# Kernel optimization log

Hardware: AMD Instinct MI355X
Metric: run time of the kernel (lower is better)

The kernel has to match this reference:

```python
import jax, jax.numpy as jnp
import numpy as np

N, E = 50000, 800000
NODE_DIM, EDGE_DIM, H = 64, 32, 128


def setup_inputs() -> dict:
    key = jax.random.key(0)
    ks = jax.random.split(key, 12)
    s = lambda fan_in: 1.0 / np.sqrt(fan_in)
    return {
        "node_feat": jax.random.normal(ks[0], (N, NODE_DIM), dtype=jnp.float32),
        "edge_index": jax.random.randint(ks[1], (2, E), 0, N, dtype=jnp.int32),
        "edge_feat": jax.random.normal(ks[2], (E, EDGE_DIM), dtype=jnp.float32),
        # node_proj: Linear(node_dim -> H)
        "W_node": jax.random.uniform(ks[3], (H, NODE_DIM), jnp.float32, -s(NODE_DIM), s(NODE_DIM)),
        "b_node": jnp.zeros((H,), jnp.float32),
        # edge_proj: Linear(edge_dim -> H)
        "W_edge": jax.random.uniform(ks[4], (H, EDGE_DIM), jnp.float32, -s(EDGE_DIM), s(EDGE_DIM)),
        "b_edge": jnp.zeros((H,), jnp.float32),
        # message: Linear(2H -> H)
        "W_msg": jax.random.uniform(ks[5], (H, 2 * H), jnp.float32, -s(2 * H), s(2 * H)),
        "b_msg": jnp.zeros((H,), jnp.float32),
        # GRUCell(H, H): weight_ih [3H,H], weight_hh [3H,H], biases [3H]
        "W_ih": jax.random.uniform(ks[6], (3 * H, H), jnp.float32, -s(H), s(H)),
        "W_hh": jax.random.uniform(ks[7], (3 * H, H), jnp.float32, -s(H), s(H)),
        "b_ih": jax.random.uniform(ks[8], (3 * H,), jnp.float32, -s(H), s(H)),
        "b_hh": jax.random.uniform(ks[9], (3 * H,), jnp.float32, -s(H), s(H)),
    }


def _gru_cell(x, h, W_ih, W_hh, b_ih, b_hh):
    # torch.nn.GRUCell semantics; gate order: reset, update, new
    gi = x @ W_ih.T + b_ih   # [N, 3H]
    gh = h @ W_hh.T + b_hh   # [N, 3H]
    i_r, i_z, i_n = jnp.split(gi, 3, axis=-1)
    h_r, h_z, h_n = jnp.split(gh, 3, axis=-1)
    r = jax.nn.sigmoid(i_r + h_r)
    z = jax.nn.sigmoid(i_z + h_z)
    n = jnp.tanh(i_n + r * h_n)
    return (1.0 - z) * n + z * h


def reference(node_feat, edge_index, edge_feat, W_node, b_node, W_edge, b_edge,
              W_msg, b_msg, W_ih, W_hh, b_ih, b_hh):
    h = node_feat @ W_node.T + b_node          # [N, H]
    e = edge_feat @ W_edge.T + b_edge          # [E, H]
    src, dst = edge_index[0], edge_index[1]
    n_nodes = h.shape[0]
    # Split the message Linear over the concat to avoid materializing [E, 2H]
    W_msg_h, W_msg_e = W_msg[:, :h.shape[1]], W_msg[:, h.shape[1]:]
    e_msg = e @ W_msg_e.T + b_msg              # edge part is loop-invariant
    for _ in range(3):
        m = h[src] @ W_msg_h.T + e_msg         # [E, H]
        agg = jax.ops.segment_sum(m, dst, num_segments=n_nodes)  # [N, H]
        h = _gru_cell(agg, h, W_ih, W_hh, b_ih, b_hh)
    return (h, e)
```

## Files before the change

kernel.cpp:

```cpp
#include <hip/hip_runtime.h>
#include <hip/hip_bf16.h>

#define NN 50000
#define EE 800000
#define ND 64
#define ED 32
#define HH 128

template<int KSTEP, bool BIAS, bool CMAT, bool DEGB>
__global__ __launch_bounds__(256) void k_gemm(
    const float* __restrict__ X, int K,
    const float* __restrict__ W, int ldw,
    const float* __restrict__ bias,
    const float* __restrict__ Cm,
    const int* __restrict__ deg,
    float* __restrict__ Y, int M, int Ncols)
{
    __shared__ float Xs[64][KSTEP + 1];
    __shared__ float Ws[64][KSTEP + 1];
    const int m0 = blockIdx.x * 64;
    const int n0 = blockIdx.y * 64;
    const int tid = threadIdx.x;
    const int tx = tid & 15, ty = tid >> 4;

    float acc[4][4] = {};

    for (int k0 = 0; k0 < K; k0 += KSTEP) {
        for (int f = tid; f < 64 * KSTEP / 4; f += 256) {
            int r = f / (KSTEP / 4);
            int c4 = (f % (KSTEP / 4)) * 4;
            int gr = m0 + r;
            float4 v = make_float4(0.f, 0.f, 0.f, 0.f);
            if (gr < M)
                v = *reinterpret_cast<const float4*>(X + (size_t)gr * K + k0 + c4);
            Xs[r][c4 + 0] = v.x; Xs[r][c4 + 1] = v.y;
            Xs[r][c4 + 2] = v.z; Xs[r][c4 + 3] = v.w;
        }
        for (int f = tid; f < 64 * KSTEP / 4; f += 256) {
            int r = f / (KSTEP / 4);
            int c4 = (f % (KSTEP / 4)) * 4;
            float4 v = *reinterpret_cast<const float4*>(W + (size_t)(n0 + r) * ldw + k0 + c4);
            Ws[r][c4 + 0] = v.x; Ws[r][c4 + 1] = v.y;
            Ws[r][c4 + 2] = v.z; Ws[r][c4 + 3] = v.w;
        }
        __syncthreads();
        #pragma unroll
        for (int kk = 0; kk < KSTEP; ++kk) {
            float a[4], b[4];
            #pragma unroll
            for (int i = 0; i < 4; ++i) a[i] = Xs[ty * 4 + i][kk];
            #pragma unroll
            for (int j = 0; j < 4; ++j) b[j] = Ws[tx * 4 + j][kk];
            #pragma unroll
            for (int i = 0; i < 4; ++i)
                #pragma unroll
                for (int j = 0; j < 4; ++j)
                    acc[i][j] += a[i] * b[j];
        }
        __syncthreads();
    }

    #pragma unroll
    for (int i = 0; i < 4; ++i) {
        int row = m0 + ty * 4 + i;
        if (row >= M) continue;
        #pragma unroll
        for (int j = 0; j < 4; ++j) {
            int col = n0 + tx * 4 + j;
            float v = acc[i][j];
            if (BIAS) v += DEGB ? bias[col] * (float)deg[row] : bias[col];
            if (CMAT) v += Cm[(size_t)row * Ncols + col];
            Y[(size_t)row * Ncols + col] = v;
        }
    }
}

__global__ __launch_bounds__(256) void k_gru(
    const float* __restrict__ hin, const float* __restrict__ Whh,
    const float* __restrict__ bhh, const float* __restrict__ gi,
    float* __restrict__ hout, int M)
{
    constexpr int KS = 32;
    __shared__ float Hs[64][KS + 1];
    __shared__ float Wr[64][KS + 1];
    __shared__ float Wz[64][KS + 1];
    __shared__ float Wn[64][KS + 1];
    const int m0 = blockIdx.x * 64;
    const int c0 = blockIdx.y * 64;
    const int tid = threadIdx.x;
    const int tx = tid & 15, ty = tid >> 4;

    float ar[4][4] = {}, az[4][4] = {}, an[4][4] = {};

    for (int k0 = 0; k0 < HH; k0 += KS) {
        for (int f = tid; f < 64 * KS / 4; f += 256) {
            int r = f / (KS / 4);
            int c4 = (f % (KS / 4)) * 4;
            int gr = m0 + r;
            float4 v = make_float4(0.f, 0.f, 0.f, 0.f);
            if (gr < M)
                v = *reinterpret_cast<const float4*>(hin + (size_t)gr * HH + k0 + c4);
            Hs[r][c4] = v.x; Hs[r][c4 + 1] = v.y; Hs[r][c4 + 2] = v.z; Hs[r][c4 + 3] = v.w;

            float4 w0 = *reinterpret_cast<const float4*>(Whh + (size_t)(c0 + r) * HH + k0 + c4);
            Wr[r][c4] = w0.x; Wr[r][c4 + 1] = w0.y; Wr[r][c4 + 2] = w0.z; Wr[r][c4 + 3] = w0.w;
            float4 w1 = *reinterpret_cast<const float4*>(Whh + (size_t)(HH + c0 + r) * HH + k0 + c4);
            Wz[r][c4] = w1.x; Wz[r][c4 + 1] = w1.y; Wz[r][c4 + 2] = w1.z; Wz[r][c4 + 3] = w1.w;
            float4 w2 = *reinterpret_cast<const float4*>(Whh + (size_t)(2 * HH + c0 + r) * HH + k0 + c4);
            Wn[r][c4] = w2.x; Wn[r][c4 + 1] = w2.y; Wn[r][c4 + 2] = w2.z; Wn[r][c4 + 3] = w2.w;
        }
        __syncthreads();
        #pragma unroll
        for (int kk = 0; kk < KS; ++kk) {
            float a[4], br[4], bz[4], bn[4];
            #pragma unroll
            for (int i = 0; i < 4; ++i) a[i] = Hs[ty * 4 + i][kk];
            #pragma unroll
            for (int j = 0; j < 4; ++j) {
                br[j] = Wr[tx * 4 + j][kk];
                bz[j] = Wz[tx * 4 + j][kk];
                bn[j] = Wn[tx * 4 + j][kk];
            }
            #pragma unroll
            for (int i = 0; i < 4; ++i)
                #pragma unroll
                for (int j = 0; j < 4; ++j) {
                    ar[i][j] += a[i] * br[j];
                    az[i][j] += a[i] * bz[j];
                    an[i][j] += a[i] * bn[j];
                }
        }
        __syncthreads();
    }

    #pragma unroll
    for (int i = 0; i < 4; ++i) {
        int row = m0 + ty * 4 + i;
        if (row >= M) continue;
        #pragma unroll
        for (int j = 0; j < 4; ++j) {
            int c = c0 + tx * 4 + j;
            float gr_ = gi[(size_t)row * 384 + c];
            float gz_ = gi[(size_t)row * 384 + HH + c];
            float gn_ = gi[(size_t)row * 384 + 2 * HH + c];
            float hr = ar[i][j] + bhh[c];
            float hz = az[i][j] + bhh[HH + c];
            float hn = an[i][j] + bhh[2 * HH + c];
            float r = 1.f / (1.f + expf(-(gr_ + hr)));
            float z = 1.f / (1.f + expf(-(gz_ + hz)));
            float n = tanhf(gn_ + r * hn);
            float hv = hin[(size_t)row * HH + c];
            hout[(size_t)row * HH + c] = (1.f - z) * n + z * hv;
        }
    }
}

__global__ void k_hist(const int* __restrict__ dst, int* __restrict__ deg, int n) {
    int e = blockIdx.x * 256 + threadIdx.x;
    if (e < n) atomicAdd(&deg[dst[e]], 1);
}

__global__ __launch_bounds__(1024) void k_scan_block(
    const int* __restrict__ deg, int* __restrict__ rp, int* __restrict__ bsum, int n)
{
    __shared__ int s[1024];
    int i = blockIdx.x * 1024 + threadIdx.x;
    s[threadIdx.x] = (i < n) ? deg[i] : 0;
    __syncthreads();
    for (int off = 1; off < 1024; off <<= 1) {
        int t = (threadIdx.x >= (unsigned)off) ? s[threadIdx.x - off] : 0;
        __syncthreads();
        s[threadIdx.x] += t;
        __syncthreads();
    }
    if (i < n) rp[i + 1] = s[threadIdx.x];
    if (threadIdx.x == 1023) bsum[blockIdx.x] = s[1023];
}

__global__ void k_scan_tops(int* bsum, int nb) {
    if (threadIdx.x == 0 && blockIdx.x == 0) {
        int run = 0;
        for (int b = 0; b < nb; ++b) { int v = bsum[b]; bsum[b] = run; run += v; }
    }
}

__global__ __launch_bounds__(1024) void k_scan_add(int* rp, const int* __restrict__ bsum, int n) {
    int i = blockIdx.x * 1024 + threadIdx.x;
    if (i < n) rp[i + 1] += bsum[blockIdx.x];
    if (i == 0) rp[0] = 0;
}

__global__ void k_cursor(const int* __restrict__ rp, int* __restrict__ cur, int n) {
    int i = blockIdx.x * 256 + threadIdx.x;
    if (i < n) cur[i] = rp[i];
}

__global__ void k_bucket(const int* __restrict__ src, const int* __restrict__ dst,
                         int* __restrict__ cur, int* __restrict__ eid,
                         int* __restrict__ ssrc, int n)
{
    int e = blockIdx.x * 256 + threadIdx.x;
    if (e < n) {
        int d = dst[e];
        int p = atomicAdd(&cur[d], 1);
        eid[p] = e;
        ssrc[p] = src[e];
    }
}

__global__ __launch_bounds__(256) void k_pull(
    const float* __restrict__ X, const int* __restrict__ idxarr,
    const int* __restrict__ rp, float* __restrict__ out, int n)
{
    int node = blockIdx.x * 4 + (threadIdx.x >> 6);
    int lane = threadIdx.x & 63;
    if (node >= n) return;
    int s = rp[node], t = rp[node + 1];
    float2 acc = make_float2(0.f, 0.f);
    for (int j = s; j < t; ++j) {
        int id = idxarr[j];
        float2 v = reinterpret_cast<const float2*>(X + (size_t)id * HH)[lane];
        acc.x += v.x; acc.y += v.y;
    }
    reinterpret_cast<float2*>(out + (size_t)node * HH)[lane] = acc;
}

extern "C" void kernel_launch(void* const* d_in, const int* in_sizes, int n_in,
                              void* d_out, int out_size, void* d_ws, size_t ws_size,
                              hipStream_t stream)
{
    const float* node_feat = (const float*)d_in[0];
    const int*   eidx      = (const int*)d_in[1];
    const float* edge_feat = (const float*)d_in[2];
    const float* W_node    = (const float*)d_in[3];
    const float* b_node    = (const float*)d_in[4];
    const float* W_edge    = (const float*)d_in[5];
    const float* b_edge    = (const float*)d_in[6];
    const float* W_msg     = (const float*)d_in[7];
    const float* b_msg     = (const float*)d_in[8];
    const float* W_ih      = (const float*)d_in[9];
    const float* W_hh      = (const float*)d_in[10];
    const float* b_ih      = (const float*)d_in[11];
    const float* b_hh      = (const float*)d_in[12];

    const int* src = eidx;
    const int* dst = eidx + EE;

    float* out_h = (float*)d_out;
    float* out_e = out_h + (size_t)NN * HH;

    float* A   = (float*)d_ws;
    float* B   = A + (size_t)NN * HH;
    float* C   = B + (size_t)NN * HH;
    float* D   = C + (size_t)NN * HH;
    float* Eb  = D + (size_t)NN * HH;
    float* F   = Eb + (size_t)NN * HH;
    int* deg   = (int*)(F + (size_t)NN * 384);
    int* rp    = deg + NN;
    int* cur   = rp + (NN + 1);
    int* bsum  = cur + NN;
    int* eid   = bsum + 64;
    int* ssrc  = eid + EE;

    hipMemsetAsync(deg, 0, NN * sizeof(int), stream);

    k_gemm<32, true, false, false><<<dim3(782, 2), 256, 0, stream>>>(
        node_feat, ND, W_node, ND, b_node, nullptr, nullptr, A, NN, HH);

    k_gemm<32, true, false, false><<<dim3(12500, 2), 256, 0, stream>>>(
        edge_feat, ED, W_edge, ED, b_edge, nullptr, nullptr, out_e, EE, HH);

    k_hist<<<EE / 256, 256, 0, stream>>>(dst, deg, EE);
    k_scan_block<<<49, 1024, 0, stream>>>(deg, rp, bsum, NN);
    k_scan_tops<<<1, 64, 0, stream>>>(bsum, 49);
    k_scan_add<<<49, 1024, 0, stream>>>(rp, bsum, NN);
    k_cursor<<<196, 256, 0, stream>>>(rp, cur, NN);
    k_bucket<<<EE / 256, 256, 0, stream>>>(src, dst, cur, eid, ssrc, EE);

    k_pull<<<12500, 256, 0, stream>>>(out_e, eid, rp, D, NN);
    k_gemm<32, true, false, true><<<dim3(782, 2), 256, 0, stream>>>(
        D, HH, W_msg + HH, 2 * HH, b_msg, nullptr, deg, C, NN, HH);

    const float* hin = A;
    for (int t = 0; t < 3; ++t) {
        float* hout = (t == 2) ? out_h : ((t == 0) ? B : A);
        k_pull<<<12500, 256, 0, stream>>>(hin, ssrc, rp, D, NN);
        k_gemm<32, false, true, false><<<dim3(782, 2), 256, 0, stream>>>(
            D, HH, W_msg, 2 * HH, nullptr, C, nullptr, Eb, NN, HH);
        k_gemm<32, true, false, false><<<dim3(782, 6), 256, 0, stream>>>(
            Eb, HH, W_ih, HH, b_ih, nullptr, nullptr, F, NN, 384);
        k_gru<<<dim3(782, 2), 256, 0, stream>>>(hin, W_hh, b_hh, F, hout, NN);
        hin = hout;
    }
}
```

Before: 1.984 ms.

## Replace FP32 SIMT GEMMs with split-bf16 MFMA GEMMs and restructure the GRU

Replaces the scalar FP32 tiled GEMM and the dedicated GRU kernel with one 128x128-tile MFMA GEMM. Each operand is split into bf16 high and low parts and three bf16 MFMAs are accumulated, approximating FP32 accuracy on matrix cores. The GRU now runs as an MFMA GEMM that adds the r/z hidden gates into F, then an n-gate GEMM with a fused sigmoid/tanh epilogue that writes h. The aim is to cut the ALU-bound GEMM cost, at the price of split-precision rounding error, an extra launch per iteration, and in-place updates of F and A whose safety depends on the access pattern (row blocks only touch their own rows).

```diff
diff --git a/kernel.cpp b/kernel.cpp
--- a/kernel.cpp
+++ b/kernel.cpp
@@ -7,150 +7,156 @@
 #define ED 32
 #define HH 128
 
-template<int KSTEP, bool BIAS, bool CMAT, bool DEGB>
-__global__ __launch_bounds__(256) void k_gemm(
+typedef __attribute__((ext_vector_type(8)))  short  bf16x8;
+typedef __attribute__((ext_vector_type(4)))  float  f32x4;
+typedef __attribute__((ext_vector_type(8)))  ushort u16x8;
+
+__device__ __forceinline__ ushort f2bf(float f) {
+    unsigned u = __float_as_uint(f);
+    unsigned r = (u + 0x7FFFu + ((u >> 16) & 1u)) >> 16;
+    return (ushort)r;
+}
+__device__ __forceinline__ float bf2f(ushort h) {
+    return __uint_as_float(((unsigned)h) << 16);
+}
+
+template<bool BIAS, bool CMAT, bool DEGB, bool GRU>
+__global__ __launch_bounds__(256) void k_mgemm(
     const float* __restrict__ X, int K,
     const float* __restrict__ W, int ldw,
     const float* __restrict__ bias,
-    const float* __restrict__ Cm,
+    const float* __restrict__ Cm, int ldc,
     const int* __restrict__ deg,
-    float* __restrict__ Y, int M, int Ncols)
-{
-    __shared__ float Xs[64][KSTEP + 1];
-    __shared__ float Ws[64][KSTEP + 1];
-    const int m0 = blockIdx.x * 64;
-    const int n0 = blockIdx.y * 64;
-    const int tid = threadIdx.x;
-    const int tx = tid & 15, ty = tid >> 4;
-
-    float acc[4][4] = {};
-
-    for (int k0 = 0; k0 < K; k0 += KSTEP) {
-        for (int f = tid; f < 64 * KSTEP / 4; f += 256) {
-            int r = f / (KSTEP / 4);
-            int c4 = (f % (KSTEP / 4)) * 4;
-            int gr = m0 + r;
-            float4 v = make_float4(0.f, 0.f, 0.f, 0.f);
-            if (gr < M)
-                v = *reinterpret_cast<const float4*>(X + (size_t)gr * K + k0 + c4);
-            Xs[r][c4 + 0] = v.x; Xs[r][c4 + 1] = v.y;
-            Xs[r][c4 + 2] = v.z; Xs[r][c4 + 3] = v.w;
-        }
-        for (int f = tid; f < 64 * KSTEP / 4; f += 256) {
-            int r = f / (KSTEP / 4);
-            int c4 = (f % (KSTEP / 4)) * 4;
-            float4 v = *reinterpret_cast<const float4*>(W + (size_t)(n0 + r) * ldw + k0 + c4);
-            Ws[r][c4 + 0] = v.x; Ws[r][c4 + 1] = v.y;
-            Ws[r][c4 + 2] = v.z; Ws[r][c4 + 3] = v.w;
+    const float* __restrict__ hprev,
+    float* __restrict__ Y, int ldy, int M)
+{
+    __shared__ ushort XH[128][40];
+    __shared__ ushort XL[128][40];
+    __shared__ ushort WH[128][40];
+    __shared__ ushort WL[128][40];
+
+    const int m0 = blockIdx.x * 128;
+    const int n0 = blockIdx.y * 128;
+    const int tid  = threadIdx.x;
+    const int lane = tid & 63;
+    const int wave = tid >> 6;
+    const int wm = wave >> 1, wn = wave & 1;
+    const int lr = lane & 15;
+    const int lg = lane >> 4;
+
+    f32x4 acc[4][4];
+    #pragma unroll
+    for (int i = 0; i < 4; ++i)
+        #pragma unroll
+        for (int j = 0; j < 4; ++j)
+            acc[i][j] = (f32x4){0.f, 0.f, 0.f, 0.f};
+
+    const int srow  = tid >> 1;
+    const int shalf = tid & 1;
+
+    for (int k0 = 0; k0 < K; k0 += 32) {
+        {
+            float v[16];
+            int gr = m0 + srow;
+            if (gr < M) {
+                const float* p = X + (size_t)gr * K + k0 + shalf * 16;
+                float4 a = *reinterpret_cast<const float4*>(p);
+                float4 b = *reinterpret_cast<const float4*>(p + 4);
+                float4 c = *reinterpret_cast<const float4*>(p + 8);
+                float4 d = *reinterpret_cast<const float4*>(p + 12);
+                v[0]=a.x; v[1]=a.y; v[2]=a.z; v[3]=a.w;
+                v[4]=b.x; v[5]=b.y; v[6]=b.z; v[7]=b.w;
+                v[8]=c.x; v[9]=c.y; v[10]=c.z; v[11]=c.w;
+                v[12]=d.x; v[13]=d.y; v[14]=d.z; v[15]=d.w;
+            } else {
+                #pragma unroll
+                for (int i = 0; i < 16; ++i) v[i] = 0.f;
+            }
+            u16x8 h0, h1, l0, l1;
+            #pragma unroll
+            for (int i = 0; i < 8; ++i) {
+                ushort h = f2bf(v[i]);      h0[i] = h; l0[i] = f2bf(v[i] - bf2f(h));
+            }
+            #pragma unroll
+            for (int i = 0; i < 8; ++i) {
+                ushort h = f2bf(v[8 + i]);  h1[i] = h; l1[i] = f2bf(v[8 + i] - bf2f(h));
+            }
+            *reinterpret_cast<u16x8*>(&XH[srow][shalf * 16])     = h0;
+            *reinterpret_cast<u16x8*>(&XH[srow][shalf * 16 + 8]) = h1;
+            *reinterpret_cast<u16x8*>(&XL[srow][shalf * 16])     = l0;
+            *reinterpret_cast<u16x8*>(&XL[srow][shalf * 16 + 8]) = l1;
+        }
+        {
+            const float* p = W + (size_t)(n0 + srow) * ldw + k0 + shalf * 16;
+            float4 a = *reinterpret_cast<const float4*>(p);
+            float4 b = *reinterpret_cast<const float4*>(p + 4);
+            float4 c = *reinterpret_cast<const float4*>(p + 8);
+            float4 d = *reinterpret_cast<const float4*>(p + 12);
+            float v[16] = {a.x,a.y,a.z,a.w, b.x,b.y,b.z,b.w,
+                           c.x,c.y,c.z,c.w, d.x,d.y,d.z,d.w};
+            u16x8 h0, h1, l0, l1;
+            #pragma unroll
+            for (int i = 0; i < 8; ++i) {
+                ushort h = f2bf(v[i]);      h0[i] = h; l0[i] = f2bf(v[i] - bf2f(h));
+            }
+            #pragma unroll
+            for (int i = 0; i < 8; ++i) {
+                ushort h = f2bf(v[8 + i]);  h1[i] = h; l1[i] = f2bf(v[8 + i] - bf2f(h));
+            }
+            *reinterpret_cast<u16x8*>(&WH[srow][shalf * 16])     = h0;
+            *reinterpret_cast<u16x8*>(&WH[srow][shalf * 16 + 8]) = h1;
+            *reinterpret_cast<u16x8*>(&WL[srow][shalf * 16])     = l0;
+            *reinterpret_cast<u16x8*>(&WL[srow][shalf * 16 + 8]) = l1;
         }
         __syncthreads();
-        #pragma unroll
-        for (int kk = 0; kk < KSTEP; ++kk) {
-            float a[4], b[4];
-            #pragma unroll
-            for (int i = 0; i < 4; ++i) a[i] = Xs[ty * 4 + i][kk];
-            #pragma unroll
-            for (int j = 0; j < 4; ++j) b[j] = Ws[tx * 4 + j][kk];
-            #pragma unroll
-            for (int i = 0; i < 4; ++i)
-                #pragma unroll
-                for (int j = 0; j < 4; ++j)
-                    acc[i][j] += a[i] * b[j];
-        }
+
+        bf16x8 ah[4], al[4], bh[4], bl[4];
+        #pragma unroll
+        for (int mf = 0; mf < 4; ++mf) {
+            ah[mf] = *reinterpret_cast<const bf16x8*>(&XH[wm * 64 + mf * 16 + lr][lg * 8]);
+            al[mf] = *reinterpret_cast<const bf16x8*>(&XL[wm * 64 + mf * 16 + lr][lg * 8]);
+        }
+        #pragma unroll
+        for (int nf = 0; nf < 4; ++nf) {
+            bh[nf] = *reinterpret_cast<const bf16x8*>(&WH[wn * 64 + nf * 16 + lr][lg * 8]);
+            bl[nf] = *reinterpret_cast<const bf16x8*>(&WL[wn * 64 + nf * 16 + lr][lg * 8]);
+        }
+        #pragma unroll
+        for (int mf = 0; mf < 4; ++mf)
+            #pragma unroll
+            for (int nf = 0; nf < 4; ++nf) {
+                acc[mf][nf] = __builtin_amdgcn_mfma_f32_16x16x32_bf16(ah[mf], bh[nf], acc[mf][nf], 0, 0, 0);
+                acc[mf][nf] = __builtin_amdgcn_mfma_f32_16x16x32_bf16(ah[mf], bl[nf], acc[mf][nf], 0, 0, 0);
+                acc[mf][nf] = __builtin_amdgcn_mfma_f32_16x16x32_bf16(al[mf], bh[nf], acc[mf][nf], 0, 0, 0);
+            }
         __syncthreads();
     }
 
     #pragma unroll
-    for (int i = 0; i < 4; ++i) {
-        int row = m0 + ty * 4 + i;
-        if (row >= M) continue;
-        #pragma unroll
-        for (int j = 0; j < 4; ++j) {
-            int col = n0 + tx * 4 + j;
-            float v = acc[i][j];
-            if (BIAS) v += DEGB ? bias[col] * (float)deg[row] : bias[col];
-            if (CMAT) v += Cm[(size_t)row * Ncols + col];
-            Y[(size_t)row * Ncols + col] = v;
-        }
-    }
-}
-
-__global__ __launch_bounds__(256) void k_gru(
-    const float* __restrict__ hin, const float* __restrict__ Whh,
-    const float* __restrict__ bhh, const float* __restrict__ gi,
-    float* __restrict__ hout, int M)
-{
-    constexpr int KS = 32;
-    __shared__ float Hs[64][KS + 1];
-    __shared__ float Wr[64][KS + 1];
-    __shared__ float Wz[64][KS + 1];
-    __shared__ float Wn[64][KS + 1];
-    const int m0 = blockIdx.x * 64;
-    const int c0 = blockIdx.y * 64;
-    const int tid = threadIdx.x;
-    const int tx = tid & 15, ty = tid >> 4;
-
-    float ar[4][4] = {}, az[4][4] = {}, an[4][4] = {};
-
-    for (int k0 = 0; k0 < HH; k0 += KS) {
-        for (int f = tid; f < 64 * KS / 4; f += 256) {
-            int r = f / (KS / 4);
-            int c4 = (f % (KS / 4)) * 4;
-            int gr = m0 + r;
-            float4 v = make_float4(0.f, 0.f, 0.f, 0.f);
-            if (gr < M)
-                v = *reinterpret_cast<const float4*>(hin + (size_t)gr * HH + k0 + c4);
-            Hs[r][c4] = v.x; Hs[r][c4 + 1] = v.y; Hs[r][c4 + 2] = v.z; Hs[r][c4 + 3] = v.w;
-
-            float4 w0 = *reinterpret_cast<const float4*>(Whh + (size_t)(c0 + r) * HH + k0 + c4);
-            Wr[r][c4] = w0.x; Wr[r][c4 + 1] = w0.y; Wr[r][c4 + 2] = w0.z; Wr[r][c4 + 3] = w0.w;
-            float4 w1 = *reinterpret_cast<const float4*>(Whh + (size_t)(HH + c0 + r) * HH + k0 + c4);
-            Wz[r][c4] = w1.x; Wz[r][c4 + 1] = w1.y; Wz[r][c4 + 2] = w1.z; Wz[r][c4 + 3] = w1.w;
-            float4 w2 = *reinterpret_cast<const float4*>(Whh + (size_t)(2 * HH + c0 + r) * HH + k0 + c4);
-            Wn[r][c4] = w2.x; Wn[r][c4 + 1] = w2.y; Wn[r][c4 + 2] = w2.z; Wn[r][c4 + 3] = w2.w;
-        }
-        __syncthreads();
-        #pragma unroll
-        for (int kk = 0; kk < KS; ++kk) {
-            float a[4], br[4], bz[4], bn[4];
-            #pragma unroll
-            for (int i = 0; i < 4; ++i) a[i] = Hs[ty * 4 + i][kk];
-            #pragma unroll
-            for (int j = 0; j < 4; ++j) {
-                br[j] = Wr[tx * 4 + j][kk];
-                bz[j] = Wz[tx * 4 + j][kk];
-                bn[j] = Wn[tx * 4 + j][kk];
-            }
-            #pragma unroll
-            for (int i = 0; i < 4; ++i)
-                #pragma unroll
-                for (int j = 0; j < 4; ++j) {
-                    ar[i][j] += a[i] * br[j];
-                    az[i][j] += a[i] * bz[j];
-                    an[i][j] += a[i] * bn[j];
+    for (int mf = 0; mf < 4; ++mf) {
+        #pragma unroll
+        for (int nf = 0; nf < 4; ++nf) {
+            int col = n0 + wn * 64 + nf * 16 + lr;
+            int rowb = m0 + wm * 64 + mf * 16 + lg * 4;
+            #pragma unroll
+            for (int i = 0; i < 4; ++i) {
+                int r = rowb + i;
+                if (r >= M) continue;
+                float v = acc[mf][nf][i];
+                if (BIAS) v += DEGB ? bias[col] * (float)deg[r] : bias[col];
+                if (GRU) {
+                    float fr = Cm[(size_t)r * ldc + col];
+                    float fz = Cm[(size_t)r * ldc + col + 128];
+                    float fn = Cm[(size_t)r * ldc + col + 256];
+                    float rr = 1.f / (1.f + expf(-fr));
+                    float zz = 1.f / (1.f + expf(-fz));
+                    float nn = tanhf(fn + rr * v);
+                    v = (1.f - zz) * nn + zz * hprev[(size_t)r * HH + col];
+                } else if (CMAT) {
+                    v += Cm[(size_t)r * ldc + col];
                 }
-        }
-        __syncthreads();
-    }
-
-    #pragma unroll
-    for (int i = 0; i < 4; ++i) {
-        int row = m0 + ty * 4 + i;
-        if (row >= M) continue;
-        #pragma unroll
-        for (int j = 0; j < 4; ++j) {
-            int c = c0 + tx * 4 + j;
-            float gr_ = gi[(size_t)row * 384 + c];
-            float gz_ = gi[(size_t)row * 384 + HH + c];
-            float gn_ = gi[(size_t)row * 384 + 2 * HH + c];
-            float hr = ar[i][j] + bhh[c];
-            float hz = az[i][j] + bhh[HH + c];
-            float hn = an[i][j] + bhh[2 * HH + c];
-            float r = 1.f / (1.f + expf(-(gr_ + hr)));
-            float z = 1.f / (1.f + expf(-(gz_ + hz)));
-            float n = tanhf(gn_ + r * hn);
-            float hv = hin[(size_t)row * HH + c];
-            hout[(size_t)row * HH + c] = (1.f - z) * n + z * hv;
+                Y[(size_t)r * ldy + col] = v;
+            }
         }
     }
 }
@@ -242,6 +248,7 @@
     const float* W_hh      = (const float*)d_in[10];
     const float* b_ih      = (const float*)d_in[11];
     const float* b_hh      = (const float*)d_in[12];
+    (void)in_sizes; (void)n_in; (void)out_size; (void)ws_size;
 
     const int* src = eidx;
     const int* dst = eidx + EE;
@@ -250,8 +257,7 @@
     float* out_e = out_h + (size_t)NN * HH;
 
     float* A   = (float*)d_ws;
-    float* B   = A + (size_t)NN * HH;
-    float* C   = B + (size_t)NN * HH;
+    float* C   = A + (size_t)NN * HH;
     float* D   = C + (size_t)NN * HH;
     float* Eb  = D + (size_t)NN * HH;
     float* F   = Eb + (size_t)NN * HH;
@@ -264,11 +270,11 @@
 
     hipMemsetAsync(deg, 0, NN * sizeof(int), stream);
 
-    k_gemm<32, true, false, false><<<dim3(782, 2), 256, 0, stream>>>(
-        node_feat, ND, W_node, ND, b_node, nullptr, nullptr, A, NN, HH);
-
-    k_gemm<32, true, false, false><<<dim3(12500, 2), 256, 0, stream>>>(
-        edge_feat, ED, W_edge, ED, b_edge, nullptr, nullptr, out_e, EE, HH);
+    k_mgemm<true, false, false, false><<<dim3(391, 1), 256, 0, stream>>>(
+        node_feat, ND, W_node, ND, b_node, nullptr, 0, nullptr, nullptr, A, HH, NN);
+
+    k_mgemm<true, false, false, false><<<dim3(6250, 1), 256, 0, stream>>>(
+        edge_feat, ED, W_edge, ED, b_edge, nullptr, 0, nullptr, nullptr, out_e, HH, EE);
 
     k_hist<<<EE / 256, 256, 0, stream>>>(dst, deg, EE);
     k_scan_block<<<49, 1024, 0, stream>>>(deg, rp, bsum, NN);
@@ -278,18 +284,19 @@
     k_bucket<<<EE / 256, 256, 0, stream>>>(src, dst, cur, eid, ssrc, EE);
 
     k_pull<<<12500, 256, 0, stream>>>(out_e, eid, rp, D, NN);
-    k_gemm<32, true, false, true><<<dim3(782, 2), 256, 0, stream>>>(
-        D, HH, W_msg + HH, 2 * HH, b_msg, nullptr, deg, C, NN, HH);
-
-    const float* hin = A;
+    k_mgemm<true, false, true, false><<<dim3(391, 1), 256, 0, stream>>>(
+        D, HH, W_msg + HH, 2 * HH, b_msg, nullptr, 0, deg, nullptr, C, HH, NN);
+
     for (int t = 0; t < 3; ++t) {
-        float* hout = (t == 2) ? out_h : ((t == 0) ? B : A);
-        k_pull<<<12500, 256, 0, stream>>>(hin, ssrc, rp, D, NN);
-        k_gemm<32, false, true, false><<<dim3(782, 2), 256, 0, stream>>>(
-            D, HH, W_msg, 2 * HH, nullptr, C, nullptr, Eb, NN, HH);
-        k_gemm<32, true, false, false><<<dim3(782, 6), 256, 0, stream>>>(
-            Eb, HH, W_ih, HH, b_ih, nullptr, nullptr, F, NN, 384);
-        k_gru<<<dim3(782, 2), 256, 0, stream>>>(hin, W_hh, b_hh, F, hout, NN);
-        hin = hout;
-    }
-}
+        float* hout = (t == 2) ? out_h : A;
+        k_pull<<<12500, 256, 0, stream>>>(A, ssrc, rp, D, NN);
+        k_mgemm<false, true, false, false><<<dim3(391, 1), 256, 0, stream>>>(
+            D, HH, W_msg, 2 * HH, nullptr, C, HH, nullptr, nullptr, Eb, HH, NN);
+        k_mgemm<true, false, false, false><<<dim3(391, 3), 256, 0, stream>>>(
+            Eb, HH, W_ih, HH, b_ih, nullptr, 0, nullptr, nullptr, F, 384, NN);
+        k_mgemm<true, true, false, false><<<dim3(391, 2), 256, 0, stream>>>(
+            A, HH, W_hh, HH, b_hh, F, 384, nullptr, nullptr, F, 384, NN);
+        k_mgemm<true, true, false, true><<<dim3(391, 1), 256, 0, stream>>>(
+            A, HH, W_hh + 256 * HH, HH, b_hh + 256, F, 384, nullptr, A, hout, HH, NN);
+    }
+}
```

Measured after the change: 1.662 ms. 1.19x faster.
